# Kernel optimization log

Measured on AMD Instinct MI355X. Metric: run time of the kernel, lower is better.

## Reference

```python
import jax, jax.numpy as jnp
import numpy as np

CE_SLICES = [(1,10),(12,29),(30,33),(33,40),(40,64),(64,79),(79,84),(84,94),(94,96),(96,99),(99,105),(105,113),(116,122),(122,128),(128,151),(151,159),(160,165)]
MSE_COLS = [0,10,11,29,113,114,115,159,165,166,167]
BINS = 800
RATIO_JSD = 0.1  # stand-in for par.RATIO_JSD (not defined in source)
B = 262144


def setup_inputs() -> dict:
    key = jax.random.key(0)
    k1, k2, k3, k4 = jax.random.split(key, 4)
    data_encoded = jax.random.normal(k1, (B, 11), dtype=jnp.float32)
    data_decoded = jax.random.normal(k2, (B, 168), dtype=jnp.float32)
    data_true = jax.random.normal(k3, (B, 168), dtype=jnp.float32)
    # categorical blocks of data_true must be one-hot (nonzero-based decode)
    for j, (s, e) in enumerate(CE_SLICES):
        lab = jax.random.randint(jax.random.fold_in(k3, j), (B,), 0, e - s)
        data_true = data_true.at[:, s:e].set(jax.nn.one_hot(lab, e - s, dtype=jnp.float32))
    label_true = jax.random.randint(k4, (B, 1), 0, 2).astype(jnp.float32)
    return {"data_encoded": data_encoded, "data_decoded": data_decoded,
            "data_true": data_true, "label_true": label_true, "batch_size": B}


def _ce(logits, labels):
    # F.cross_entropy with mean reduction
    logp = jax.nn.log_softmax(logits, axis=-1)
    return -jnp.mean(jnp.take_along_axis(logp, labels[:, None], axis=1))


def _hist(x, mn, mx, mask):
    # torch.histc semantics: BINS equal bins on [mn, mx], top edge inclusive.
    t = (x - mn) / (mx - mn)
    idx = jnp.clip(jnp.floor(t * BINS).astype(jnp.int32), 0, BINS - 1)
    return jax.ops.segment_sum(mask, idx, num_segments=BINS)


def _kl(p, q, eps=1e-12):
    return jnp.sum(jnp.where(p > 0, p * jnp.log((p + eps) / (q + eps)), 0.0))


def reference(data_encoded, data_decoded, data_true, label_true, batch_size):
    # ---- MSE losses over 11 scalar columns (vectorized) ----
    cols = jnp.array(MSE_COLS)
    diff = data_decoded[:, cols] - data_true[:, cols]            # [B, 11]
    mse_loss = jnp.sum(jnp.mean(diff * diff, axis=0))

    # ---- 17 cross-entropy heads (labels decoded from one-hot blocks) ----
    ce_loss = jnp.float32(0.0)
    for s, e in CE_SLICES:
        labels = jnp.argmax(data_true[:, s:e], axis=1)           # == first nonzero for one-hot
        ce_loss = ce_loss + _ce(data_decoded[:, s:e], labels)

    # ---- JSD between male/female histograms of first 10 encoded dims ----
    combined = jnp.concatenate([data_encoded, label_true], axis=1)  # [B, 12]
    mn = jnp.min(combined, axis=0)
    mx = jnp.max(combined, axis=0)
    male = (combined[:, 11] == 0).astype(jnp.float32)
    female = (combined[:, 11] == 1).astype(jnp.float32)
    cols10 = combined[:, :10].T                                  # [10, B]
    hist = jax.vmap(_hist, in_axes=(0, 0, 0, None))              # [10, BINS]
    m_h = hist(cols10, mn[:10], mx[:10], male) / jnp.sum(male)
    f_h = hist(cols10, mn[:10], mx[:10], female) / jnp.sum(female)
    mid = 0.5 * (m_h + f_h)
    kld = 0.5 * (_kl(m_h, mid) + _kl(f_h, mid))                  # Jensen-Shannon divergence

    multi = (1.0 - RATIO_JSD) * (mse_loss + ce_loss) + RATIO_JSD * kld
    return jnp.stack([multi, mse_loss, ce_loss, RATIO_JSD * kld])
```

## Files before the change

### kernel.cpp

```cpp
#include <hip/hip_runtime.h>
#include <math.h>


#define BINS 800
#define NHCOLS 10

#define MIN_OFF 0
#define MAX_OFF 16
#define CNT_OFF 32
#define SUM_OFF 34
#define MH_OFF  64
#define FH_OFF  8064
#define WS_U32_TOTAL 16064

__device__ __forceinline__ unsigned f2ord(float f) {
  unsigned u = __float_as_uint(f);
  return (u & 0x80000000u) ? ~u : (u | 0x80000000u);
}
__device__ __forceinline__ float ord2f(unsigned e) {
  return __uint_as_float((e & 0x80000000u) ? (e & 0x7FFFFFFFu) : ~e);
}

__global__ void k_init(unsigned* __restrict__ ws) {
  int i = blockIdx.x * blockDim.x + threadIdx.x;
  if (i < WS_U32_TOTAL) ws[i] = (i < 11) ? 0xFFFFFFFFu : 0u;
}

__global__ __launch_bounds__(256) void k_minmax(const float* __restrict__ enc,
                                                const float* __restrict__ lab,
                                                unsigned* __restrict__ ws, int B) {
  const int tid    = blockIdx.x * blockDim.x + threadIdx.x;
  const int stride = gridDim.x * blockDim.x;
  const int c      = tid % 11;
  unsigned mn = 0xFFFFFFFFu, mx = 0u;
  const long long total = (long long)B * 11;
  for (long long i = tid; i < total; i += stride) {
    unsigned e = f2ord(enc[i]);
    mn = mn < e ? mn : e;
    mx = mx > e ? mx : e;
  }
  __shared__ unsigned smn[11], smx[11], scnt[2];
  if (threadIdx.x < 11) { smn[threadIdx.x] = 0xFFFFFFFFu; smx[threadIdx.x] = 0u; }
  if (threadIdx.x < 2)  scnt[threadIdx.x] = 0u;
  __syncthreads();
  atomicMin(&smn[c], mn);
  atomicMax(&smx[c], mx);
  unsigned m = 0, f = 0;
  for (int i = tid; i < B; i += stride) {
    float v = lab[i];
    m += (v == 0.0f);
    f += (v == 1.0f);
  }
  atomicAdd(&scnt[0], m);
  atomicAdd(&scnt[1], f);
  __syncthreads();
  if (threadIdx.x < 11) {
    atomicMin(&ws[MIN_OFF + threadIdx.x], smn[threadIdx.x]);
    atomicMax(&ws[MAX_OFF + threadIdx.x], smx[threadIdx.x]);
  }
  if (threadIdx.x == 11) atomicAdd(&ws[CNT_OFF + 0], scnt[0]);
  if (threadIdx.x == 12) atomicAdd(&ws[CNT_OFF + 1], scnt[1]);
}

__global__ __launch_bounds__(256) void k_hist(const float* __restrict__ enc,
                                              const float* __restrict__ lab,
                                              unsigned* __restrict__ ws, int B) {
  __shared__ unsigned h[NHCOLS * BINS];
  for (int i = threadIdx.x; i < NHCOLS * BINS; i += blockDim.x) h[i] = 0u;
  float mn[NHCOLS], rng[NHCOLS];
#pragma unroll
  for (int c = 0; c < NHCOLS; ++c) {
    float lo = ord2f(ws[MIN_OFF + c]);
    float hi = ord2f(ws[MAX_OFF + c]);
    mn[c] = lo; rng[c] = hi - lo;
  }
  __syncthreads();
  const int tid    = blockIdx.x * blockDim.x + threadIdx.x;
  const int stride = gridDim.x * blockDim.x;
  for (int r = tid; r < B; r += stride) {
    float lv = lab[r];
    unsigned add = (lv == 0.0f) ? 1u : ((lv == 1.0f) ? 0x10000u : 0u);
    if (add) {
      const float* row = enc + (long long)r * 11;
#pragma unroll
      for (int c = 0; c < NHCOLS; ++c) {
        float t = (row[c] - mn[c]) / rng[c];
        int b = (int)floorf(t * 800.0f);
        b = b < 0 ? 0 : (b > BINS - 1 ? BINS - 1 : b);
        atomicAdd(&h[c * BINS + b], add);
      }
    }
  }
  __syncthreads();
  for (int i = threadIdx.x; i < NHCOLS * BINS; i += blockDim.x) {
    unsigned v = h[i];
    unsigned lo = v & 0xFFFFu, hi = v >> 16;
    if (lo) atomicAdd(&ws[MH_OFF + i], lo);
    if (hi) atomicAdd(&ws[FH_OFF + i], hi);
  }
}

template<int S, int E>
__device__ __forceinline__ float ce_slice(const float* __restrict__ dR,
                                          const float* __restrict__ tR) {
  constexpr int W = E - S;
  float d[W];
  float m = -3.402823466e38f;
#pragma unroll
  for (int j = 0; j < W; ++j) { d[j] = dR[S + j]; m = fmaxf(m, d[j]); }
  float dot = 0.0f;
#pragma unroll
  for (int j = 0; j < W; ++j) dot = fmaf(tR[S + j], d[j], dot);
  float s = 0.0f;
#pragma unroll
  for (int j = 0; j < W; ++j) s += __expf(d[j] - m);
  return m + __logf(s) - dot;
}

__global__ __launch_bounds__(256) void k_main(const float* __restrict__ dec,
                                              const float* __restrict__ tru,
                                              float* __restrict__ wsf, int B) {
  int r = blockIdx.x * blockDim.x + threadIdx.x;
  float mse = 0.0f, ce = 0.0f;
  if (r < B) {
    const float* dR = dec + (long long)r * 168;
    const float* tR = tru + (long long)r * 168;
#define MSEC(c) { float df = dR[c] - tR[c]; mse = fmaf(df, df, mse); }
    MSEC(0)
    ce += ce_slice<1, 10>(dR, tR);
    MSEC(10) MSEC(11)
    ce += ce_slice<12, 29>(dR, tR);
    MSEC(29)
    ce += ce_slice<30, 33>(dR, tR);
    ce += ce_slice<33, 40>(dR, tR);
    ce += ce_slice<40, 64>(dR, tR);
    ce += ce_slice<64, 79>(dR, tR);
    ce += ce_slice<79, 84>(dR, tR);
    ce += ce_slice<84, 94>(dR, tR);
    ce += ce_slice<94, 96>(dR, tR);
    ce += ce_slice<96, 99>(dR, tR);
    ce += ce_slice<99, 105>(dR, tR);
    ce += ce_slice<105, 113>(dR, tR);
    MSEC(113) MSEC(114) MSEC(115)
    ce += ce_slice<116, 122>(dR, tR);
    ce += ce_slice<122, 128>(dR, tR);
    ce += ce_slice<128, 151>(dR, tR);
    ce += ce_slice<151, 159>(dR, tR);
    MSEC(159)
    ce += ce_slice<160, 165>(dR, tR);
    MSEC(165) MSEC(166) MSEC(167)
#undef MSEC
  }
  __shared__ float sm[4], sc[4];
  int lane = threadIdx.x & 63, wid = threadIdx.x >> 6;
#pragma unroll
  for (int off = 32; off > 0; off >>= 1) {
    mse += __shfl_down(mse, off, 64);
    ce  += __shfl_down(ce, off, 64);
  }
  if (lane == 0) { sm[wid] = mse; sc[wid] = ce; }
  __syncthreads();
  if (threadIdx.x == 0) {
    atomicAdd(&wsf[SUM_OFF + 0], sm[0] + sm[1] + sm[2] + sm[3]);
    atomicAdd(&wsf[SUM_OFF + 1], sc[0] + sc[1] + sc[2] + sc[3]);
  }
}

__global__ __launch_bounds__(256) void k_final(const unsigned* __restrict__ ws,
                                               float* __restrict__ out, int B) {
  const float* wsf = (const float*)ws;
  float male   = (float)ws[CNT_OFF + 0];
  float female = (float)ws[CNT_OFF + 1];
  float local = 0.0f;
  for (int i = threadIdx.x; i < NHCOLS * BINS; i += blockDim.x) {
    float mh  = (float)ws[MH_OFF + i] / male;
    float fh  = (float)ws[FH_OFF + i] / female;
    float mid = 0.5f * (mh + fh);
    if (mh > 0.0f) local += mh * logf((mh + 1e-12f) / (mid + 1e-12f));
    if (fh > 0.0f) local += fh * logf((fh + 1e-12f) / (mid + 1e-12f));
  }
  __shared__ float s[4];
  int lane = threadIdx.x & 63, wid = threadIdx.x >> 6;
#pragma unroll
  for (int off = 32; off > 0; off >>= 1) local += __shfl_down(local, off, 64);
  if (lane == 0) s[wid] = local;
  __syncthreads();
  if (threadIdx.x == 0) {
    float kld   = 0.5f * (s[0] + s[1] + s[2] + s[3]);
    float mse   = wsf[SUM_OFF + 0] / (float)B;
    float ce    = wsf[SUM_OFF + 1] / (float)B;
    float multi = 0.9f * (mse + ce) + 0.1f * kld;
    out[0] = multi;
    out[1] = mse;
    out[2] = ce;
    out[3] = 0.1f * kld;
  }
}

extern "C" void kernel_launch(void* const* d_in, const int* in_sizes, int n_in,
                              void* d_out, int out_size, void* d_ws, size_t ws_size,
                              hipStream_t stream) {
  (void)n_in; (void)out_size; (void)ws_size;
  const float* enc = (const float*)d_in[0];
  const float* dec = (const float*)d_in[1];
  const float* tru = (const float*)d_in[2];
  const float* lab = (const float*)d_in[3];
  const int B = in_sizes[3];
  unsigned* ws = (unsigned*)d_ws;
  float* out = (float*)d_out;

  hipLaunchKernelGGL(k_init, dim3((WS_U32_TOTAL + 255) / 256), dim3(256), 0, stream, ws);
  hipLaunchKernelGGL(k_minmax, dim3(352), dim3(256), 0, stream, enc, lab, ws, B);
  hipLaunchKernelGGL(k_hist, dim3(128), dim3(256), 0, stream, enc, lab, ws, B);
  hipLaunchKernelGGL(k_main, dim3((B + 255) / 256), dim3(256), 0, stream,
                     dec, tru, (float*)ws, B);
  hipLaunchKernelGGL(k_final, dim3(1), dim3(256), 0, stream, ws, out, B);
}
```

Measured before the change: 496.3 us.

## Coalesce row loads with 4-lane float4 split and privatize histogram partials

The main loss kernel now assigns four lanes per row, loading float4 vectors so global reads are coalesced, and computes softmax max/sum/dot via cross-lane xor shuffles with predicated columns. The histogram kernel uses two shared sub-histograms per block to cut LDS atomic contention and writes per-block partials, which a new merge kernel reduces instead of using global atomics. The workspace init shrinks accordingly. This raises register pressure in the main kernel and adds one extra launch plus a partial buffer read.

```diff
diff --git a/kernel.cpp b/kernel.cpp
--- a/kernel.cpp
+++ b/kernel.cpp
@@ -4,6 +4,7 @@
 
 #define BINS 800
 #define NHCOLS 10
+#define HB 128
 
 #define MIN_OFF 0
 #define MAX_OFF 16
@@ -11,7 +12,8 @@
 #define SUM_OFF 34
 #define MH_OFF  64
 #define FH_OFF  8064
-#define WS_U32_TOTAL 16064
+#define PART_OFF 16384
+#define WS_INIT_U32 64
 
 __device__ __forceinline__ unsigned f2ord(float f) {
   unsigned u = __float_as_uint(f);
@@ -23,7 +25,7 @@
 
 __global__ void k_init(unsigned* __restrict__ ws) {
   int i = blockIdx.x * blockDim.x + threadIdx.x;
-  if (i < WS_U32_TOTAL) ws[i] = (i < 11) ? 0xFFFFFFFFu : 0u;
+  if (i < WS_INIT_U32) ws[i] = (i < 11) ? 0xFFFFFFFFu : 0u;
 }
 
 __global__ __launch_bounds__(256) void k_minmax(const float* __restrict__ enc,
@@ -65,8 +67,9 @@
 __global__ __launch_bounds__(256) void k_hist(const float* __restrict__ enc,
                                               const float* __restrict__ lab,
                                               unsigned* __restrict__ ws, int B) {
-  __shared__ unsigned h[NHCOLS * BINS];
-  for (int i = threadIdx.x; i < NHCOLS * BINS; i += blockDim.x) h[i] = 0u;
+  __shared__ unsigned h[2][NHCOLS * BINS];
+  unsigned* hf = &h[0][0];
+  for (int i = threadIdx.x; i < 2 * NHCOLS * BINS; i += blockDim.x) hf[i] = 0u;
   float mn[NHCOLS], rng[NHCOLS];
 #pragma unroll
   for (int c = 0; c < NHCOLS; ++c) {
@@ -75,9 +78,8 @@
     mn[c] = lo; rng[c] = hi - lo;
   }
   __syncthreads();
-  const int tid    = blockIdx.x * blockDim.x + threadIdx.x;
-  const int stride = gridDim.x * blockDim.x;
-  for (int r = tid; r < B; r += stride) {
+  const int sub = (threadIdx.x >> 6) & 1;
+  for (int r = blockIdx.x * 256 + threadIdx.x; r < B; r += HB * 256) {
     float lv = lab[r];
     unsigned add = (lv == 0.0f) ? 1u : ((lv == 1.0f) ? 0x10000u : 0u);
     if (add) {
@@ -87,72 +89,130 @@
         float t = (row[c] - mn[c]) / rng[c];
         int b = (int)floorf(t * 800.0f);
         b = b < 0 ? 0 : (b > BINS - 1 ? BINS - 1 : b);
-        atomicAdd(&h[c * BINS + b], add);
+        atomicAdd(&h[sub][c * BINS + b], add);
       }
     }
   }
   __syncthreads();
-  for (int i = threadIdx.x; i < NHCOLS * BINS; i += blockDim.x) {
-    unsigned v = h[i];
-    unsigned lo = v & 0xFFFFu, hi = v >> 16;
-    if (lo) atomicAdd(&ws[MH_OFF + i], lo);
-    if (hi) atomicAdd(&ws[FH_OFF + i], hi);
-  }
-}
-
-template<int S, int E>
-__device__ __forceinline__ float ce_slice(const float* __restrict__ dR,
-                                          const float* __restrict__ tR) {
-  constexpr int W = E - S;
-  float d[W];
-  float m = -3.402823466e38f;
-#pragma unroll
-  for (int j = 0; j < W; ++j) { d[j] = dR[S + j]; m = fmaxf(m, d[j]); }
-  float dot = 0.0f;
-#pragma unroll
-  for (int j = 0; j < W; ++j) dot = fmaf(tR[S + j], d[j], dot);
+  for (int i = threadIdx.x; i < NHCOLS * BINS; i += blockDim.x)
+    ws[PART_OFF + blockIdx.x * (NHCOLS * BINS) + i] = h[0][i] + h[1][i];
+}
+
+__global__ __launch_bounds__(256) void k_merge(unsigned* __restrict__ ws) {
+  int i = blockIdx.x * blockDim.x + threadIdx.x;
+  if (i >= NHCOLS * BINS) return;
+  unsigned m = 0, f = 0;
+  for (int p = 0; p < HB; ++p) {
+    unsigned v = ws[PART_OFF + p * (NHCOLS * BINS) + i];
+    m += v & 0xFFFFu;
+    f += v >> 16;
+  }
+  ws[MH_OFF + i] = m;
+  ws[FH_OFF + i] = f;
+}
+
+
+template<int A, int E>
+__device__ __forceinline__ float ce_slice3(const float (&d)[11][4],
+                                           const float (&t)[11][4], int j) {
+  constexpr int W0 = A >> 4;
+  constexpr int W1 = (E - 1) >> 4;
+  float m = -3.402823466e38f, dot = 0.0f;
+#pragma unroll
+  for (int i = W0; i <= W1; ++i) {
+#pragma unroll
+    for (int k = 0; k < 4; ++k) {
+      int c = 16 * i + 4 * j + k;
+      bool p = (c >= A) && (c < E);
+      float v = d[i][k];
+      m   = p ? fmaxf(m, v) : m;
+      dot = p ? fmaf(t[i][k], v, dot) : dot;
+    }
+  }
+  m = fmaxf(m, __shfl_xor(m, 1, 64));
+  m = fmaxf(m, __shfl_xor(m, 2, 64));
   float s = 0.0f;
 #pragma unroll
-  for (int j = 0; j < W; ++j) s += __expf(d[j] - m);
+  for (int i = W0; i <= W1; ++i) {
+#pragma unroll
+    for (int k = 0; k < 4; ++k) {
+      int c = 16 * i + 4 * j + k;
+      bool p = (c >= A) && (c < E);
+      s += __expf(p ? (d[i][k] - m) : -88.0f);
+    }
+  }
+  s   += __shfl_xor(s, 1, 64);
+  s   += __shfl_xor(s, 2, 64);
+  dot += __shfl_xor(dot, 1, 64);
+  dot += __shfl_xor(dot, 2, 64);
   return m + __logf(s) - dot;
+}
+
+template<int C>
+__device__ __forceinline__ float mse_col(const float (&d)[11][4],
+                                         const float (&t)[11][4], int j) {
+  constexpr int I = C >> 4, K = C & 3, J = (C >> 2) & 3;
+  float df = d[I][K] - t[I][K];
+  return (j == J) ? df * df : 0.0f;
 }
 
 __global__ __launch_bounds__(256) void k_main(const float* __restrict__ dec,
                                               const float* __restrict__ tru,
                                               float* __restrict__ wsf, int B) {
-  int r = blockIdx.x * blockDim.x + threadIdx.x;
-  float mse = 0.0f, ce = 0.0f;
-  if (r < B) {
-    const float* dR = dec + (long long)r * 168;
-    const float* tR = tru + (long long)r * 168;
-#define MSEC(c) { float df = dR[c] - tR[c]; mse = fmaf(df, df, mse); }
-    MSEC(0)
-    ce += ce_slice<1, 10>(dR, tR);
-    MSEC(10) MSEC(11)
-    ce += ce_slice<12, 29>(dR, tR);
-    MSEC(29)
-    ce += ce_slice<30, 33>(dR, tR);
-    ce += ce_slice<33, 40>(dR, tR);
-    ce += ce_slice<40, 64>(dR, tR);
-    ce += ce_slice<64, 79>(dR, tR);
-    ce += ce_slice<79, 84>(dR, tR);
-    ce += ce_slice<84, 94>(dR, tR);
-    ce += ce_slice<94, 96>(dR, tR);
-    ce += ce_slice<96, 99>(dR, tR);
-    ce += ce_slice<99, 105>(dR, tR);
-    ce += ce_slice<105, 113>(dR, tR);
-    MSEC(113) MSEC(114) MSEC(115)
-    ce += ce_slice<116, 122>(dR, tR);
-    ce += ce_slice<122, 128>(dR, tR);
-    ce += ce_slice<128, 151>(dR, tR);
-    ce += ce_slice<151, 159>(dR, tR);
-    MSEC(159)
-    ce += ce_slice<160, 165>(dR, tR);
-    MSEC(165) MSEC(166) MSEC(167)
-#undef MSEC
-  }
+  const int lane = threadIdx.x & 63;
+  const int wid  = threadIdx.x >> 6;
+  const int j    = lane & 3;
+  const int row  = blockIdx.x * 64 + (wid << 4) + (lane >> 2);
+  const bool valid = row < B;
+
+  float d[11][4], t[11][4];
+  const float4* d4 = (const float4*)(dec + (size_t)row * 168);
+  const float4* t4 = (const float4*)(tru + (size_t)row * 168);
+#pragma unroll
+  for (int i = 0; i < 11; ++i) {
+    const int w = 4 * i + j;
+    float4 dv = make_float4(0.f, 0.f, 0.f, 0.f);
+    float4 tv = make_float4(0.f, 0.f, 0.f, 0.f);
+    if (valid && w < 42) { dv = d4[w]; tv = t4[w]; }
+    d[i][0] = dv.x; d[i][1] = dv.y; d[i][2] = dv.z; d[i][3] = dv.w;
+    t[i][0] = tv.x; t[i][1] = tv.y; t[i][2] = tv.z; t[i][3] = tv.w;
+  }
+
+  float ce = 0.0f, mse = 0.0f;
+  ce += ce_slice3<1, 10>(d, t, j);
+  ce += ce_slice3<12, 29>(d, t, j);
+  ce += ce_slice3<30, 33>(d, t, j);
+  ce += ce_slice3<33, 40>(d, t, j);
+  ce += ce_slice3<40, 64>(d, t, j);
+  ce += ce_slice3<64, 79>(d, t, j);
+  ce += ce_slice3<79, 84>(d, t, j);
+  ce += ce_slice3<84, 94>(d, t, j);
+  ce += ce_slice3<94, 96>(d, t, j);
+  ce += ce_slice3<96, 99>(d, t, j);
+  ce += ce_slice3<99, 105>(d, t, j);
+  ce += ce_slice3<105, 113>(d, t, j);
+  ce += ce_slice3<116, 122>(d, t, j);
+  ce += ce_slice3<122, 128>(d, t, j);
+  ce += ce_slice3<128, 151>(d, t, j);
+  ce += ce_slice3<151, 159>(d, t, j);
+  ce += ce_slice3<160, 165>(d, t, j);
+
+  mse += mse_col<0>(d, t, j);
+  mse += mse_col<10>(d, t, j);
+  mse += mse_col<11>(d, t, j);
+  mse += mse_col<29>(d, t, j);
+  mse += mse_col<113>(d, t, j);
+  mse += mse_col<114>(d, t, j);
+  mse += mse_col<115>(d, t, j);
+  mse += mse_col<159>(d, t, j);
+  mse += mse_col<165>(d, t, j);
+  mse += mse_col<166>(d, t, j);
+  mse += mse_col<167>(d, t, j);
+
+  ce  = (valid && j == 0) ? ce : 0.0f;
+  mse = valid ? mse : 0.0f;
+
   __shared__ float sm[4], sc[4];
-  int lane = threadIdx.x & 63, wid = threadIdx.x >> 6;
 #pragma unroll
   for (int off = 32; off > 0; off >>= 1) {
     mse += __shfl_down(mse, off, 64);
@@ -209,10 +269,11 @@
   unsigned* ws = (unsigned*)d_ws;
   float* out = (float*)d_out;
 
-  hipLaunchKernelGGL(k_init, dim3((WS_U32_TOTAL + 255) / 256), dim3(256), 0, stream, ws);
+  hipLaunchKernelGGL(k_init, dim3(1), dim3(64), 0, stream, ws);
   hipLaunchKernelGGL(k_minmax, dim3(352), dim3(256), 0, stream, enc, lab, ws, B);
-  hipLaunchKernelGGL(k_hist, dim3(128), dim3(256), 0, stream, enc, lab, ws, B);
-  hipLaunchKernelGGL(k_main, dim3((B + 255) / 256), dim3(256), 0, stream,
+  hipLaunchKernelGGL(k_hist, dim3(HB), dim3(256), 0, stream, enc, lab, ws, B);
+  hipLaunchKernelGGL(k_merge, dim3((NHCOLS * BINS + 255) / 256), dim3(256), 0, stream, ws);
+  hipLaunchKernelGGL(k_main, dim3((B + 63) / 64), dim3(256), 0, stream,
                      dec, tru, (float*)ws, B);
   hipLaunchKernelGGL(k_final, dim3(1), dim3(256), 0, stream, ws, out, B);
 }
```

Result: faster. 456.0 us (-8.1%).
